# Optimization experiments

Hardware: AMD Instinct MI355X
Metric: run time of the kernel (lower is better)

Reference implementation:

```python
import jax, jax.numpy as jnp
import numpy as np

VOCAB = 128
HID = 128
SEQ = 65536


def setup_inputs() -> dict:
    key = jax.random.key(0)
    ks = jax.random.split(key, 12)
    u = lambda k, shape, s: jax.random.uniform(k, shape, jnp.float32, -s, s)
    sA = 1.0 / np.sqrt(VOCAB)
    sH = 1.0 / np.sqrt(HID)
    return {
        "x": jax.random.normal(ks[0], (1, SEQ, VOCAB), jnp.float32),
        "hA": jnp.zeros((1, HID), jnp.float32),
        "cA": jnp.zeros((1, HID), jnp.float32),
        "hB": jnp.zeros((1, HID), jnp.float32),
        "cB": jnp.zeros((1, HID), jnp.float32),
        "WA1": u(ks[1], (4 * HID, VOCAB), sA), "bA1": u(ks[2], (4 * HID,), sA),
        "WA2": u(ks[3], (4 * HID, HID), sH), "bA2": u(ks[4], (4 * HID,), sH),
        "WB1": u(ks[5], (4 * HID, HID), sH), "bB1": u(ks[6], (4 * HID,), sH),
        "WB2": u(ks[7], (4 * HID, HID), sH), "bB2": u(ks[8], (4 * HID,), sH),
        # init_weights(): fc.weight ~ U(-1,1), fc.bias = 0
        "Wfc": jax.random.uniform(ks[9], (VOCAB, HID), jnp.float32, -1.0, 1.0),
        "bfc": jnp.zeros((VOCAB,), jnp.float32),
    }


def _lstm_cell(x_in, h, c, W1, b1, W2, b2):
    gates = x_in @ W1.T + b1 + h @ W2.T + b2  # [1, 4H]
    i, f, g, o = jnp.split(gates, 4, axis=-1)
    c = jax.nn.sigmoid(f) * c + jax.nn.sigmoid(i) * jnp.tanh(g)
    h = jax.nn.sigmoid(o) * jnp.tanh(c)
    return h, c


def reference(x, hA, cA, hB, cB, WA1, bA1, WA2, bA2, WB1, bB1, WB2, bB2, Wfc, bfc):
    # original takes x.unbind(0)[0] -> iterate over timesteps of batch element 0
    inputs = x[0][:, None, :]  # [S, 1, V]

    def step(carry, xt):
        hA, cA, hB, cB = carry
        hA, cA = _lstm_cell(xt, hA, cA, WA1, bA1, WA2, bA2)
        hB, cB = _lstm_cell(hA, hB, cB, WB1, bB1, WB2, bB2)
        return (hA, cA, hB, cB), hB

    (hA, cA, hB, cB), outs = jax.lax.scan(step, (hA, cA, hB, cB), inputs)
    # dropout is identity in eval; reshape [S,1,H] -> [S*1,H], then fc
    logits = outs.reshape(-1, HID) @ Wfc.T + bfc  # [S, VOCAB]
    return logits, hA, cA, hB, cB
```

## Files before the change

kernel.cpp:

```cpp
#include <hip/hip_runtime.h>

typedef unsigned short u16;
typedef unsigned int   u32;
typedef __bf16 bf16x8 __attribute__((ext_vector_type(8)));
typedef float  f32x4  __attribute__((ext_vector_type(4)));

#define T_SEQ 65536

__device__ __forceinline__ float bf2f(u16 v){ return __uint_as_float(((u32)v) << 16); }
__device__ __forceinline__ float bflo(u32 w){ return __uint_as_float(w << 16); }
__device__ __forceinline__ float bfhi(u32 w){ return __uint_as_float(w & 0xFFFF0000u); }
__device__ __forceinline__ u16 f2bf(float f){
  u32 u = __float_as_uint(f);
  u32 r = (u + 0x7FFFu + ((u >> 16) & 1u)) >> 16;
  return (u16)r;
}
__device__ __forceinline__ float sigm(float x){ return 1.0f / (1.0f + __expf(-x)); }
__device__ __forceinline__ float tanh_(float x){ return 1.0f - 2.0f / (1.0f + __expf(2.0f * x)); }

__device__ __forceinline__ float ldf(const void* p, size_t i, int f){
  return f ? ((const float*)p)[i] : bf2f(((const u16*)p)[i]);
}
__device__ __forceinline__ void stf(void* p, size_t i, float v, int f){
  if (f) ((float*)p)[i] = v; else ((u16*)p)[i] = f2bf(v);
}

__device__ __forceinline__ bf16x8 ldg_frag(const u16* p){
  uint4 v = *(const uint4*)p;
  return __builtin_bit_cast(bf16x8, v);
}
__device__ __forceinline__ bf16x8 load_frag_dyn(const void* p, int off, int f){
  if (!f) return ldg_frag((const u16*)p + off);
  union { u16 h[8]; bf16x8 v; } t;
  const float* q = (const float*)p + off;
#pragma unroll
  for (int j = 0; j < 8; ++j) t.h[j] = f2bf(q[j]);
  return t.v;
}
__device__ __forceinline__ bf16x8 lds_frag(const u16* p){
  uint4 v = *(const uint4*)p;
  return __builtin_bit_cast(bf16x8, v);
}

__device__ __forceinline__ void bar_sync(){
  asm volatile("s_waitcnt lgkmcnt(0)" ::: "memory");
  __builtin_amdgcn_s_barrier();
  asm volatile("" ::: "memory");
}

struct Ptrs { const void* p[15]; int n[15]; };

__global__ void k_detect(Ptrs ptrs, int* flags){
  const int i = threadIdx.x;
  if (i >= 15) return;
  const u32* w = (const u32*)ptrs.p[i];
  int words = ptrs.n[i] >> 1; if (words > 256) words = 256;
  int bad = 0, good = 0;
  for (int j = 0; j < words; ++j){
    u32 lo = w[j] & 0xFFFFu;
    if (lo == 0) continue;
    u32 e = (lo >> 7) & 0xFFu;
    if (e >= 96 && e <= 135) ++good; else ++bad;
  }
  flags[i] = (bad > good) ? 1 : 0;
}

__global__ __launch_bounds__(512) void k_gemm(const void* __restrict__ in, const void* __restrict__ W,
                                              const void* __restrict__ b1, const void* __restrict__ b2,
                                              const int* __restrict__ flags,
                                              int fiIn, int fiW, int fiB1, int fiB2,
                                              u16* __restrict__ out, int tbase){
  __shared__ __align__(16) float sx[32 * 128];
  const int fin = (fiIn < 0) ? 0 : flags[fiIn];
  const int fw = flags[fiW], f1 = flags[fiB1], f2 = flags[fiB2];
  const int tid = threadIdx.x;
  const int tl0 = blockIdx.x * 32;
  const int tg0 = tbase + tl0;
  for (int i = tid; i < 32 * 128; i += 512) sx[i] = ldf(in, (size_t)tg0 * 128 + i, fin);
  __syncthreads();
  const int r = tid;
  float bias = ldf(b1, r, f1) + ldf(b2, r, f2);
  float acc[32];
#pragma unroll
  for (int t = 0; t < 32; ++t) acc[t] = bias;
  if (!fw){
    const u32* wrow = (const u32*)W + r * 64;
    for (int c = 0; c < 32; ++c){
      uint2 wp = *(const uint2*)(wrow + 2 * c);
      float w0 = bflo(wp.x), w1 = bfhi(wp.x), w2 = bflo(wp.y), w3 = bfhi(wp.y);
#pragma unroll
      for (int t = 0; t < 32; ++t){
        const f32x4 xv = *(const f32x4*)&sx[t * 128 + 4 * c];
        acc[t] += w0 * xv.x + w1 * xv.y + w2 * xv.z + w3 * xv.w;
      }
    }
  } else {
    const float* wrow = (const float*)W + r * 128;
    for (int c = 0; c < 32; ++c){
      const f32x4 wv = *(const f32x4*)(wrow + 4 * c);
#pragma unroll
      for (int t = 0; t < 32; ++t){
        const f32x4 xv = *(const f32x4*)&sx[t * 128 + 4 * c];
        acc[t] += wv.x * xv.x + wv.y * xv.y + wv.z * xv.z + wv.w * xv.w;
      }
    }
  }
  for (int t = 0; t < 32; ++t) out[(size_t)(tl0 + t) * 512 + r] = f2bf(acc[t]);
}

__global__ __launch_bounds__(512, 2) void k_dual(
    const u16* __restrict__ preA, u16* __restrict__ preB,
    u16* __restrict__ hAws, u16* __restrict__ hb,
    const void* __restrict__ WA2, const void* __restrict__ WB1, const void* __restrict__ WB2,
    const void* __restrict__ hA0, const void* __restrict__ cA0,
    const void* __restrict__ hB0, const void* __restrict__ cB0,
    const void* __restrict__ bB1, const void* __restrict__ bB2,
    const int* __restrict__ flags, u32* __restrict__ flagA, u32* __restrict__ flagP,
    u16* __restrict__ stH, float* __restrict__ stC,
    void* __restrict__ outBase, int first, int last, int L)
{
  __shared__ __align__(16) u16 sPre[2][16 * 512];
  __shared__ __align__(16) u16 sH[2][128];

  const int tid = threadIdx.x;
  const int w = tid >> 6, l = tid & 63, q = l >> 4, m = l & 15;
  const int fo = flags[0];
  const int role = blockIdx.x;
  const int G = L >> 4;

  if (role == 1){
    const int fW = flags[9], f1 = flags[10], f2 = flags[12];
    bf16x8 wf[4][4];
#pragma unroll
    for (int rt = 0; rt < 4; ++rt){
      const int row = (w * 4 + rt) * 16 + m;
#pragma unroll
      for (int kt = 0; kt < 4; ++kt)
        wf[rt][kt] = load_frag_dyn(WB1, row * 128 + kt * 32 + q * 8, fW);
    }
    float bias[4][4];
#pragma unroll
    for (int rt = 0; rt < 4; ++rt)
#pragma unroll
      for (int rg = 0; rg < 4; ++rg){
        const int r = (w * 4 + rt) * 16 + q * 4 + rg;
        bias[rt][rg] = ldf(bB1, r, f1) + ldf(bB2, r, f2);
      }
    for (int g = 0; g < G; ++g){
      if (tid == 0){
        while (atomicAdd(&flagA[g], 0u) == 0u) __builtin_amdgcn_s_sleep(8);
      }
      __syncthreads();
      const u16* hg = hAws + (size_t)g * 2048;
      f32x4 acc[4];
#pragma unroll
      for (int rt = 0; rt < 4; ++rt) acc[rt] = (f32x4){0.f, 0.f, 0.f, 0.f};
#pragma unroll
      for (int kt = 0; kt < 4; ++kt){
        bf16x8 bfrag = ldg_frag(hg + m * 128 + kt * 32 + q * 8);
#pragma unroll
        for (int rt = 0; rt < 4; ++rt)
          acc[rt] = __builtin_amdgcn_mfma_f32_16x16x32_bf16(wf[rt][kt], bfrag, acc[rt], 0, 0, 0);
      }
      const int tg = g * 16 + m;
#pragma unroll
      for (int rt = 0; rt < 4; ++rt){
        ushort4 o;
        o.x = f2bf(acc[rt].x + bias[rt][0]);
        o.y = f2bf(acc[rt].y + bias[rt][1]);
        o.z = f2bf(acc[rt].z + bias[rt][2]);
        o.w = f2bf(acc[rt].w + bias[rt][3]);
        *(ushort4*)(preB + (size_t)tg * 512 + (w * 4 + rt) * 16 + q * 4) = o;
      }
      __threadfence();
      __syncthreads();
      if (tid == 0) atomicExch(&flagP[g], 1u);
    }
    return;
  }

  const bool isA = (role == 0);
  const u16* pre = isA ? preA : preB;
  u16* hdump = isA ? hAws : hb;
  const void* Wm = isA ? WA2 : WB2;
  const void* h0 = isA ? hA0 : hB0;
  const void* c0 = isA ? cA0 : cB0;
  const int fW  = isA ? flags[7] : flags[11];
  const int fH0 = isA ? flags[1] : flags[3];
  const int fC0 = isA ? flags[2] : flags[4];
  const int sto = isA ? 0 : 128;

  bf16x8 wf[4][4];
#pragma unroll
  for (int rt = 0; rt < 4; ++rt){
    const int row = rt * 128 + w * 16 + m;
#pragma unroll
    for (int kt = 0; kt < 4; ++kt)
      wf[rt][kt] = load_frag_dyn(Wm, row * 128 + kt * 32 + q * 8, fW);
  }

  const int j = w * 16 + m;
  float c;
  if (first){
    c = ldf(c0, j, fC0);
    if (tid < 128) sH[0][tid] = f2bf(ldf(h0, tid, fH0));
  } else {
    c = stC[sto + j];
    if (tid < 128) sH[0][tid] = stH[sto + tid];
  }

  if (!isA){
    if (tid == 0){
      while (atomicAdd(&flagP[0], 0u) == 0u) __builtin_amdgcn_s_sleep(8);
    }
    __syncthreads();
  }
  {
    const uint4* src = (const uint4*)pre;
    uint4* dst = (uint4*)&sPre[0][0];
    dst[tid]       = src[tid];
    dst[tid + 512] = src[tid + 512];
  }
  __syncthreads();

  uint4 st0, st1;
  int pend = 0, pbuf = 0;
  u16 hq = 0;

  for (int t = 0; t < L; ++t){
    const int slot = t & 15;
    const int g = t >> 4;
    const int buf = g & 1;
    const int rb = t & 1;

    if (slot == 0){
      if (isA){
        if (g > 0) __threadfence();
        const int nc = g + 1;
        if (nc < G){
          const uint4* src = (const uint4*)pre;
          st0 = src[(size_t)nc * 1024 + tid];
          st1 = src[(size_t)nc * 1024 + 512 + tid];
          pend = 1; pbuf = nc & 1;
        }
      }
    } else if (slot == 1){
      if (isA){
        if (g > 0 && tid == 448) atomicExch(&flagA[g - 1], 1u);
      } else {
        const int nc = g + 1;
        if (nc < G){
          if (tid == 0){
            while (atomicAdd(&flagP[nc], 0u) == 0u) __builtin_amdgcn_s_sleep(8);
          }
          bar_sync();
          const uint4* src = (const uint4*)(pre + (size_t)nc * 8192);
          st0 = src[tid];
          st1 = src[tid + 512];
          pend = 1; pbuf = nc & 1;
        }
      }
    } else if (slot == 2){
      if (pend){
        uint4* dst = (uint4*)&sPre[pbuf][0];
        dst[tid]       = st0;
        dst[tid + 512] = st1;
        pend = 0;
      }
    }

    const u16* pc = &sPre[buf][slot * 512 + j];
    const float pp0 = bf2f(pc[0]);
    const float pp1 = bf2f(pc[128]);
    const float pp2 = bf2f(pc[256]);
    const float pp3 = bf2f(pc[384]);

    bf16x8 bh[4];
#pragma unroll
    for (int kt = 0; kt < 4; ++kt) bh[kt] = lds_frag(&sH[rb][kt * 32 + q * 8]);

    f32x4 acc[4];
#pragma unroll
    for (int rt = 0; rt < 4; ++rt) acc[rt] = (f32x4){0.f, 0.f, 0.f, 0.f};
#pragma unroll
    for (int kt = 0; kt < 4; ++kt)
#pragma unroll
      for (int rt = 0; rt < 4; ++rt)
        acc[rt] = __builtin_amdgcn_mfma_f32_16x16x32_bf16(bh[kt], wf[rt][kt], acc[rt], 0, 0, 0);

    const float gi = sigm (pp0 + acc[0].x);
    const float gf = sigm (pp1 + acc[1].x);
    const float gg = tanh_(pp2 + acc[2].x);
    const float go = sigm (pp3 + acc[3].x);
    c = gf * c + gi * gg;
    hq = f2bf(go * tanh_(c));
    if (q == 0){
      sH[rb ^ 1][j] = hq;
      hdump[(size_t)t * 128 + j] = hq;
    }
    bar_sync();
  }

  if (isA) __threadfence();
  __syncthreads();
  if (isA && tid == 0) atomicExch(&flagA[G - 1], 1u);
  if (q == 0){
    stC[sto + j] = c;
    stH[sto + j] = hq;
    if (last){
      const size_t ob = (size_t)T_SEQ * 128;
      const size_t hOff = isA ? 0 : 256;
      const size_t cOff = isA ? 128 : 384;
      stf(outBase, ob + hOff + j, bf2f(hq), fo);
      stf(outBase, ob + cOff + j, c,        fo);
    }
  }
}

__global__ __launch_bounds__(256) void k_fc(const u16* __restrict__ hb,
                                            const void* __restrict__ Wfc, const void* __restrict__ bfc,
                                            const int* __restrict__ flags,
                                            void* __restrict__ out, int t0){
  __shared__ __align__(16) float sh[32 * 128];
  const int fw = flags[13], fb = flags[14], fo = flags[0];
  const int tid = threadIdx.x;
  const int tl0 = blockIdx.x * 32;
  for (int i = tid; i < 32 * 128; i += 256) sh[i] = bf2f(hb[(size_t)tl0 * 128 + i]);
  __syncthreads();
  const int v  = tid & 127;
  const int tt = tid >> 7;
  float bias = ldf(bfc, v, fb);
  float acc[16];
#pragma unroll
  for (int j = 0; j < 16; ++j) acc[j] = bias;
  if (!fw){
    const u32* wrow = (const u32*)Wfc + v * 64;
    for (int c = 0; c < 32; ++c){
      uint2 wp = *(const uint2*)(wrow + 2 * c);
      float w0 = bflo(wp.x), w1 = bfhi(wp.x), w2 = bflo(wp.y), w3 = bfhi(wp.y);
#pragma unroll
      for (int j = 0; j < 16; ++j){
        const f32x4 xv = *(const f32x4*)&sh[(tt + 2 * j) * 128 + 4 * c];
        acc[j] += w0 * xv.x + w1 * xv.y + w2 * xv.z + w3 * xv.w;
      }
    }
  } else {
    const float* wrow = (const float*)Wfc + v * 128;
    for (int c = 0; c < 32; ++c){
      const f32x4 wv = *(const f32x4*)(wrow + 4 * c);
#pragma unroll
      for (int j = 0; j < 16; ++j){
        const f32x4 xv = *(const f32x4*)&sh[(tt + 2 * j) * 128 + 4 * c];
        acc[j] += wv.x * xv.x + wv.y * xv.y + wv.z * xv.z + wv.w * xv.w;
      }
    }
  }
  for (int j = 0; j < 16; ++j)
    stf(out, (size_t)(t0 + tl0 + tt + 2 * j) * 128 + v, acc[j], fo);
}

extern "C" void kernel_launch(void* const* d_in, const int* in_sizes, int n_in,
                              void* d_out, int out_size, void* d_ws, size_t ws_size,
                              hipStream_t stream) {
  int CHUNK = 32;
  size_t dataOff = 4096;
  for (int c = T_SEQ; c >= 32; c >>= 1){
    size_t G = (size_t)c / 16;
    size_t dOff = (2048 + 8 * G + 4095) & ~(size_t)4095;
    size_t need = dOff + (size_t)c * 2560;
    if (need <= ws_size){ CHUNK = c; dataOff = dOff; break; }
  }
  const size_t G = (size_t)CHUNK / 16;
  float* stC    = (float*)d_ws;
  u16*   stH    = (u16*)((char*)d_ws + 1024);
  int*   dflags = (int*)((char*)d_ws + 1536);
  u32*   flagA  = (u32*)((char*)d_ws + 2048);
  u32*   flagP  = (u32*)((char*)d_ws + 2048 + 4 * G);
  u16*   preA   = (u16*)((char*)d_ws + dataOff);
  u16*   preB   = (u16*)((char*)d_ws + dataOff + (size_t)CHUNK * 1024);
  u16*   hAws   = (u16*)((char*)d_ws + dataOff + (size_t)CHUNK * 2048);
  u16*   hb     = (u16*)((char*)d_ws + dataOff + (size_t)CHUNK * 2048 + (size_t)CHUNK * 256);

  Ptrs ptrs;
  for (int i = 0; i < 15; ++i){ ptrs.p[i] = d_in[i]; ptrs.n[i] = in_sizes[i]; }
  k_detect<<<1, 64, 0, stream>>>(ptrs, dflags);

  const int nChunks = T_SEQ / CHUNK;
  for (int c = 0; c < nChunks; ++c){
    const int t0 = c * CHUNK;
    const int first = (c == 0), last = (c == nChunks - 1);
    hipMemsetAsync(flagA, 0, 8 * G, stream);
    k_gemm<<<CHUNK / 32, 512, 0, stream>>>(d_in[0], d_in[5], d_in[6], d_in[8], dflags,
                                           0, 5, 6, 8, preA, t0);
    k_dual<<<3, 512, 0, stream>>>(preA, preB, hAws, hb,
                                  d_in[7], d_in[9], d_in[11],
                                  d_in[1], d_in[2], d_in[3], d_in[4],
                                  d_in[10], d_in[12],
                                  dflags, flagA, flagP, stH, stC,
                                  d_out, first, last, CHUNK);
    k_fc  <<<CHUNK / 32, 256, 0, stream>>>(hb, d_in[13], d_in[14], dflags, d_out, t0);
  }
}
```

Before: 59.24 ms.

## Halve recurrent LSTM blocks to 256 threads with two hidden units per lane

The sequential LSTM recurrence kernel drops from 512 to 256 threads per block. Each wavefront now handles two 16-row hidden tiles, which doubles the weight fragments held in registers, while the B-input projection role does 8 row tiles per wave. Preactivations are stored gate-interleaved so each lane reads its four gate values with one 8-byte LDS load. Flag signalling and fences move to separate slots, and spin-waits get a timeout abort. The aim is to cut per-step barrier cost and LDS traffic on the latency-bound serial loop, at the cost of more MFMA and transcendental work per lane and higher register pressure.

```diff
diff --git a/kernel.cpp b/kernel.cpp
--- a/kernel.cpp
+++ b/kernel.cpp
@@ -79,6 +79,7 @@
   for (int i = tid; i < 32 * 128; i += 512) sx[i] = ldf(in, (size_t)tg0 * 128 + i, fin);
   __syncthreads();
   const int r = tid;
+  const int rr = ((r & 127) << 2) | (r >> 7);
   float bias = ldf(b1, r, f1) + ldf(b2, r, f2);
   float acc[32];
 #pragma unroll
@@ -105,10 +106,10 @@
       }
     }
   }
-  for (int t = 0; t < 32; ++t) out[(size_t)(tl0 + t) * 512 + r] = f2bf(acc[t]);
-}
-
-__global__ __launch_bounds__(512, 2) void k_dual(
+  for (int t = 0; t < 32; ++t) out[(size_t)(tl0 + t) * 512 + rr] = f2bf(acc[t]);
+}
+
+__global__ __launch_bounds__(256, 1) void k_dual(
     const u16* __restrict__ preA, u16* __restrict__ preB,
     u16* __restrict__ hAws, u16* __restrict__ hb,
     const void* __restrict__ WA2, const void* __restrict__ WB1, const void* __restrict__ WB2,
@@ -121,57 +122,64 @@
 {
   __shared__ __align__(16) u16 sPre[2][16 * 512];
   __shared__ __align__(16) u16 sH[2][128];
+  __shared__ u32 sAbort;
 
   const int tid = threadIdx.x;
   const int w = tid >> 6, l = tid & 63, q = l >> 4, m = l & 15;
   const int fo = flags[0];
   const int role = blockIdx.x;
   const int G = L >> 4;
+  const unsigned long long PTO = 200000ull;
+
+  if (tid == 0) sAbort = 0u;
 
   if (role == 1){
     const int fW = flags[9], f1 = flags[10], f2 = flags[12];
-    bf16x8 wf[4][4];
-#pragma unroll
-    for (int rt = 0; rt < 4; ++rt){
-      const int row = (w * 4 + rt) * 16 + m;
+    bf16x8 wf[8][4];
+#pragma unroll
+    for (int rt = 0; rt < 8; ++rt){
+      const int row = (w * 8 + rt) * 16 + m;
 #pragma unroll
       for (int kt = 0; kt < 4; ++kt)
         wf[rt][kt] = load_frag_dyn(WB1, row * 128 + kt * 32 + q * 8, fW);
     }
-    float bias[4][4];
-#pragma unroll
-    for (int rt = 0; rt < 4; ++rt)
+    float bias[8][4];
+#pragma unroll
+    for (int rt = 0; rt < 8; ++rt)
 #pragma unroll
       for (int rg = 0; rg < 4; ++rg){
-        const int r = (w * 4 + rt) * 16 + q * 4 + rg;
+        const int r = (w * 8 + rt) * 16 + q * 4 + rg;
         bias[rt][rg] = ldf(bB1, r, f1) + ldf(bB2, r, f2);
       }
     for (int g = 0; g < G; ++g){
-      if (tid == 0){
-        while (atomicAdd(&flagA[g], 0u) == 0u) __builtin_amdgcn_s_sleep(8);
+      if (tid == 0 && sAbort == 0u){
+        const unsigned long long tt0 = __builtin_amdgcn_s_memrealtime();
+        while (atomicAdd(&flagA[g], 0u) == 0u){
+          __builtin_amdgcn_s_sleep(8);
+          if (__builtin_amdgcn_s_memrealtime() - tt0 > PTO){ sAbort = 1u; break; }
+        }
       }
       __syncthreads();
       const u16* hg = hAws + (size_t)g * 2048;
-      f32x4 acc[4];
-#pragma unroll
-      for (int rt = 0; rt < 4; ++rt) acc[rt] = (f32x4){0.f, 0.f, 0.f, 0.f};
+      f32x4 acc[8];
+#pragma unroll
+      for (int rt = 0; rt < 8; ++rt) acc[rt] = (f32x4){0.f, 0.f, 0.f, 0.f};
 #pragma unroll
       for (int kt = 0; kt < 4; ++kt){
         bf16x8 bfrag = ldg_frag(hg + m * 128 + kt * 32 + q * 8);
 #pragma unroll
-        for (int rt = 0; rt < 4; ++rt)
+        for (int rt = 0; rt < 8; ++rt)
           acc[rt] = __builtin_amdgcn_mfma_f32_16x16x32_bf16(wf[rt][kt], bfrag, acc[rt], 0, 0, 0);
       }
       const int tg = g * 16 + m;
 #pragma unroll
-      for (int rt = 0; rt < 4; ++rt){
-        ushort4 o;
-        o.x = f2bf(acc[rt].x + bias[rt][0]);
-        o.y = f2bf(acc[rt].y + bias[rt][1]);
-        o.z = f2bf(acc[rt].z + bias[rt][2]);
-        o.w = f2bf(acc[rt].w + bias[rt][3]);
-        *(ushort4*)(preB + (size_t)tg * 512 + (w * 4 + rt) * 16 + q * 4) = o;
-      }
+      for (int rt = 0; rt < 8; ++rt)
+#pragma unroll
+        for (int rg = 0; rg < 4; ++rg){
+          const int r = (w * 8 + rt) * 16 + q * 4 + rg;
+          preB[(size_t)tg * 512 + (((r & 127) << 2) | (r >> 7))] =
+              f2bf(acc[rt][rg] + bias[rt][rg]);
+        }
       __threadfence();
       __syncthreads();
       if (tid == 0) atomicExch(&flagP[g], 1u);
@@ -190,42 +198,51 @@
   const int fC0 = isA ? flags[2] : flags[4];
   const int sto = isA ? 0 : 128;
 
-  bf16x8 wf[4][4];
-#pragma unroll
-  for (int rt = 0; rt < 4; ++rt){
-    const int row = rt * 128 + w * 16 + m;
-#pragma unroll
-    for (int kt = 0; kt < 4; ++kt)
-      wf[rt][kt] = load_frag_dyn(Wm, row * 128 + kt * 32 + q * 8, fW);
-  }
-
-  const int j = w * 16 + m;
-  float c;
+  bf16x8 wf[2][4][4];
+#pragma unroll
+  for (int ti = 0; ti < 2; ++ti)
+#pragma unroll
+    for (int rt = 0; rt < 4; ++rt){
+      const int row = rt * 128 + (w * 2 + ti) * 16 + m;
+#pragma unroll
+      for (int kt = 0; kt < 4; ++kt)
+        wf[ti][rt][kt] = load_frag_dyn(Wm, row * 128 + kt * 32 + q * 8, fW);
+    }
+
+  const int j0 = (w * 2) * 16 + m;
+  const int j1 = j0 + 16;
+  float c0_, c1_;
   if (first){
-    c = ldf(c0, j, fC0);
+    c0_ = ldf(c0, j0, fC0);
+    c1_ = ldf(c0, j1, fC0);
     if (tid < 128) sH[0][tid] = f2bf(ldf(h0, tid, fH0));
   } else {
-    c = stC[sto + j];
+    c0_ = stC[sto + j0];
+    c1_ = stC[sto + j1];
     if (tid < 128) sH[0][tid] = stH[sto + tid];
   }
 
   if (!isA){
-    if (tid == 0){
-      while (atomicAdd(&flagP[0], 0u) == 0u) __builtin_amdgcn_s_sleep(8);
+    if (tid == 0 && sAbort == 0u){
+      const unsigned long long tt0 = __builtin_amdgcn_s_memrealtime();
+      while (atomicAdd(&flagP[0], 0u) == 0u){
+        __builtin_amdgcn_s_sleep(8);
+        if (__builtin_amdgcn_s_memrealtime() - tt0 > PTO){ sAbort = 1u; break; }
+      }
     }
     __syncthreads();
   }
   {
     const uint4* src = (const uint4*)pre;
     uint4* dst = (uint4*)&sPre[0][0];
-    dst[tid]       = src[tid];
-    dst[tid + 512] = src[tid + 512];
+#pragma unroll
+    for (int i = 0; i < 4; ++i) dst[tid + 256 * i] = src[tid + 256 * i];
   }
   __syncthreads();
 
-  uint4 st0, st1;
+  uint4 st[4];
   int pend = 0, pbuf = 0;
-  u16 hq = 0;
+  u16 hq0 = 0, hq1 = 0;
 
   for (int t = 0; t < L; ++t){
     const int slot = t & 15;
@@ -235,68 +252,86 @@
 
     if (slot == 0){
       if (isA){
-        if (g > 0) __threadfence();
         const int nc = g + 1;
         if (nc < G){
           const uint4* src = (const uint4*)pre;
-          st0 = src[(size_t)nc * 1024 + tid];
-          st1 = src[(size_t)nc * 1024 + 512 + tid];
+#pragma unroll
+          for (int i = 0; i < 4; ++i) st[i] = src[(size_t)nc * 1024 + tid + 256 * i];
           pend = 1; pbuf = nc & 1;
         }
       }
     } else if (slot == 1){
-      if (isA){
-        if (g > 0 && tid == 448) atomicExch(&flagA[g - 1], 1u);
-      } else {
+      if (!isA){
         const int nc = g + 1;
         if (nc < G){
-          if (tid == 0){
-            while (atomicAdd(&flagP[nc], 0u) == 0u) __builtin_amdgcn_s_sleep(8);
+          if (tid == 0 && sAbort == 0u){
+            const unsigned long long tt0 = __builtin_amdgcn_s_memrealtime();
+            while (atomicAdd(&flagP[nc], 0u) == 0u){
+              __builtin_amdgcn_s_sleep(8);
+              if (__builtin_amdgcn_s_memrealtime() - tt0 > PTO){ sAbort = 1u; break; }
+            }
           }
           bar_sync();
           const uint4* src = (const uint4*)(pre + (size_t)nc * 8192);
-          st0 = src[tid];
-          st1 = src[tid + 512];
+#pragma unroll
+          for (int i = 0; i < 4; ++i) st[i] = src[tid + 256 * i];
           pend = 1; pbuf = nc & 1;
         }
       }
     } else if (slot == 2){
       if (pend){
         uint4* dst = (uint4*)&sPre[pbuf][0];
-        dst[tid]       = st0;
-        dst[tid + 512] = st1;
+#pragma unroll
+        for (int i = 0; i < 4; ++i) dst[tid + 256 * i] = st[i];
         pend = 0;
       }
-    }
-
-    const u16* pc = &sPre[buf][slot * 512 + j];
-    const float pp0 = bf2f(pc[0]);
-    const float pp1 = bf2f(pc[128]);
-    const float pp2 = bf2f(pc[256]);
-    const float pp3 = bf2f(pc[384]);
+    } else if (slot == 3){
+      if (isA && g > 0) __threadfence();
+    } else if (slot == 4){
+      if (isA && g > 0 && tid == 192) atomicExch(&flagA[g - 1], 1u);
+    }
+
+    const uint2 pw0 = *(const uint2*)&sPre[buf][slot * 512 + j0 * 4];
+    const uint2 pw1 = *(const uint2*)&sPre[buf][slot * 512 + j1 * 4];
 
     bf16x8 bh[4];
 #pragma unroll
     for (int kt = 0; kt < 4; ++kt) bh[kt] = lds_frag(&sH[rb][kt * 32 + q * 8]);
 
-    f32x4 acc[4];
-#pragma unroll
-    for (int rt = 0; rt < 4; ++rt) acc[rt] = (f32x4){0.f, 0.f, 0.f, 0.f};
+    f32x4 acc[2][4];
+#pragma unroll
+    for (int ti = 0; ti < 2; ++ti)
+#pragma unroll
+      for (int rt = 0; rt < 4; ++rt) acc[ti][rt] = (f32x4){0.f, 0.f, 0.f, 0.f};
 #pragma unroll
     for (int kt = 0; kt < 4; ++kt)
 #pragma unroll
-      for (int rt = 0; rt < 4; ++rt)
-        acc[rt] = __builtin_amdgcn_mfma_f32_16x16x32_bf16(bh[kt], wf[rt][kt], acc[rt], 0, 0, 0);
-
-    const float gi = sigm (pp0 + acc[0].x);
-    const float gf = sigm (pp1 + acc[1].x);
-    const float gg = tanh_(pp2 + acc[2].x);
-    const float go = sigm (pp3 + acc[3].x);
-    c = gf * c + gi * gg;
-    hq = f2bf(go * tanh_(c));
+      for (int ti = 0; ti < 2; ++ti)
+#pragma unroll
+        for (int rt = 0; rt < 4; ++rt)
+          acc[ti][rt] = __builtin_amdgcn_mfma_f32_16x16x32_bf16(bh[kt], wf[ti][rt][kt], acc[ti][rt], 0, 0, 0);
+
+    {
+      const float gi = sigm (bflo(pw0.x) + acc[0][0].x);
+      const float gf = sigm (bfhi(pw0.x) + acc[0][1].x);
+      const float gg = tanh_(bflo(pw0.y) + acc[0][2].x);
+      const float go = sigm (bfhi(pw0.y) + acc[0][3].x);
+      c0_ = gf * c0_ + gi * gg;
+      hq0 = f2bf(go * tanh_(c0_));
+    }
+    {
+      const float gi = sigm (bflo(pw1.x) + acc[1][0].x);
+      const float gf = sigm (bfhi(pw1.x) + acc[1][1].x);
+      const float gg = tanh_(bflo(pw1.y) + acc[1][2].x);
+      const float go = sigm (bfhi(pw1.y) + acc[1][3].x);
+      c1_ = gf * c1_ + gi * gg;
+      hq1 = f2bf(go * tanh_(c1_));
+    }
     if (q == 0){
-      sH[rb ^ 1][j] = hq;
-      hdump[(size_t)t * 128 + j] = hq;
+      sH[rb ^ 1][j0] = hq0;
+      sH[rb ^ 1][j1] = hq1;
+      hdump[(size_t)t * 128 + j0] = hq0;
+      hdump[(size_t)t * 128 + j1] = hq1;
     }
     bar_sync();
   }
@@ -305,14 +340,16 @@
   __syncthreads();
   if (isA && tid == 0) atomicExch(&flagA[G - 1], 1u);
   if (q == 0){
-    stC[sto + j] = c;
-    stH[sto + j] = hq;
+    stC[sto + j0] = c0_;  stC[sto + j1] = c1_;
+    stH[sto + j0] = hq0;  stH[sto + j1] = hq1;
     if (last){
       const size_t ob = (size_t)T_SEQ * 128;
       const size_t hOff = isA ? 0 : 256;
       const size_t cOff = isA ? 128 : 384;
-      stf(outBase, ob + hOff + j, bf2f(hq), fo);
-      stf(outBase, ob + cOff + j, c,        fo);
+      stf(outBase, ob + hOff + j0, bf2f(hq0), fo);
+      stf(outBase, ob + hOff + j1, bf2f(hq1), fo);
+      stf(outBase, ob + cOff + j0, c0_,       fo);
+      stf(outBase, ob + cOff + j1, c1_,       fo);
     }
   }
 }
@@ -392,7 +429,7 @@
     hipMemsetAsync(flagA, 0, 8 * G, stream);
     k_gemm<<<CHUNK / 32, 512, 0, stream>>>(d_in[0], d_in[5], d_in[6], d_in[8], dflags,
                                            0, 5, 6, 8, preA, t0);
-    k_dual<<<3, 512, 0, stream>>>(preA, preB, hAws, hb,
+    k_dual<<<3, 256, 0, stream>>>(preA, preB, hAws, hb,
                                   d_in[7], d_in[9], d_in[11],
                                   d_in[1], d_in[2], d_in[3], d_in[4],
                                   d_in[10], d_in[12],
```

Measured after the change: 57.81 ms, median of 2. 2.4% less time.
